# Kernel optimization log

Measured on AMD Instinct MI355X. Metric: run time of the kernel, lower is better.

Reference implementation:

```python
import jax, jax.numpy as jnp
import numpy as np

N_OSC = 2048
N_SAMPLES = 2 ** 14  # hard-coded in the original module
PI = float(np.pi)


def setup_inputs() -> dict:
    key = jax.random.key(0)
    k1, k2 = jax.random.split(key)
    # matches torch.zeros(n_osc, 2).uniform_(0.0001, 0.99999)
    params = jax.random.uniform(k1, (N_OSC, 2), minval=1e-4, maxval=0.99999, dtype=jnp.float32)
    # x is accepted by forward but unused by the math
    x = jax.random.normal(k2, (1, N_SAMPLES), dtype=jnp.float32)
    return {"x": x, "params": params}


def reference(x, params):
    # mode == 'complex':
    #   amp  = ||params||_2 along dim=1  (reassigned BEFORE freq is computed)
    #   freq = angle(amp + i * params[:, 0]) / pi
    amp = jnp.linalg.norm(params, axis=1)                      # (n_osc,)
    freq = jnp.arctan2(params[:, 0], amp) / PI                 # (n_osc,)
    # cumsum of a constant along the sample axis == (i+1) * freq, but we keep
    # the cumsum form to match the original op-for-op.
    accum = jnp.broadcast_to(freq[None, :, None], (1, N_OSC, N_SAMPLES))
    phase = jnp.cumsum(accum, axis=-1) * PI                    # (1, n_osc, n_samples)
    signal = (amp[None, :, None] * jnp.sin(phase)).sum(axis=1)  # (1, n_samples)
    return signal
```

## Files before the change

kernel.cpp:

```cpp
#include <hip/hip_runtime.h>
#include <math.h>

#define N_OSC 2048
#define N_SAMP 16384
#define CHUNKS 16
#define OPC (N_OSC / CHUNKS)

__global__ __launch_bounds__(256) void synth_fused(const float* __restrict__ params,
                                                   float* __restrict__ partial) {
    __shared__ float sh_hi[OPC];
    __shared__ float sh_lo[OPC];
    __shared__ float sh_amp[OPC];

    const int tx = threadIdx.x;
    const int o0 = blockIdx.y * OPC;

    if (tx < OPC) {
        double p0  = (double)params[2 * (o0 + tx) + 0];
        double p1  = (double)params[2 * (o0 + tx) + 1];
        double a   = sqrt(p0 * p0 + p1 * p1);
        double rev = atan2(p0, a) * 0.15915494309189535;
        float hi = (float)rev;
        hi = __uint_as_float(__float_as_uint(hi) & 0xFFFFC000u);
        sh_hi[tx]  = hi;
        sh_lo[tx]  = (float)(rev - (double)hi);
        sh_amp[tx] = (float)a;
    }
    __syncthreads();

    const int s = blockIdx.x * 256 + tx;
    const float sp1 = (float)(s + 1);

    float acc0 = 0.f, acc1 = 0.f;
#pragma unroll 8
    for (int i = 0; i < OPC; i += 2) {
        float uh0 = sp1 * sh_hi[i + 0];
        float uh1 = sp1 * sh_hi[i + 1];
        float t0  = __builtin_amdgcn_fractf(uh0);
        float t1  = __builtin_amdgcn_fractf(uh1);
        float r0  = __builtin_amdgcn_fractf(fmaf(sp1, sh_lo[i + 0], t0));
        float r1  = __builtin_amdgcn_fractf(fmaf(sp1, sh_lo[i + 1], t1));
        acc0 = fmaf(sh_amp[i + 0], __builtin_amdgcn_sinf(r0), acc0);
        acc1 = fmaf(sh_amp[i + 1], __builtin_amdgcn_sinf(r1), acc1);
    }
    partial[blockIdx.y * N_SAMP + s] = acc0 + acc1;
}

__global__ __launch_bounds__(256) void reduce_kernel(const float* __restrict__ partial,
                                                     float* __restrict__ out) {
    int s = blockIdx.x * 256 + threadIdx.x;
    float acc = 0.f;
#pragma unroll
    for (int c = 0; c < CHUNKS; ++c) acc += partial[c * N_SAMP + s];
    out[s] = acc;
}

__global__ __launch_bounds__(256) void inline_kernel(const float* __restrict__ params,
                                                     float* __restrict__ out) {
    int s = blockIdx.x * 256 + threadIdx.x;
    if (s >= N_SAMP) return;
    const double sp1 = (double)(s + 1);
    double acc = 0.0;
    for (int o = 0; o < N_OSC; ++o) {
        double p0 = (double)params[2 * o + 0];
        double p1 = (double)params[2 * o + 1];
        double a  = sqrt(p0 * p0 + p1 * p1);
        double u  = sp1 * (atan2(p0, a) * 0.15915494309189535);
        float  r  = (float)(u - floor(u));
        acc += a * (double)__builtin_amdgcn_sinf(r);
    }
    out[s] = (float)acc;
}

extern "C" void kernel_launch(void* const* d_in, const int* in_sizes, int n_in,
                              void* d_out, int out_size, void* d_ws, size_t ws_size,
                              hipStream_t stream) {
    const float* params = (const float*)d_in[1];
    float* out = (float*)d_out;

    const size_t part_bytes = (size_t)CHUNKS * N_SAMP * sizeof(float);

    if (ws_size >= part_bytes) {
        float* partial = (float*)d_ws;
        synth_fused<<<dim3(N_SAMP / 256, CHUNKS), 256, 0, stream>>>(params, partial);
        reduce_kernel<<<N_SAMP / 256, 256, 0, stream>>>(partial, out);
    } else {
        inline_kernel<<<N_SAMP / 256, 256, 0, stream>>>(params, out);
    }
}
```

Measured before the change: 14.15 us.

## Fuse chunked synthesis and reduction into one kernel with fp32 phase

Replaces the two-kernel scheme (partial sums to workspace, then a reduce kernel) with one kernel where 16 oscillator chunks per block reduce through shared memory. Oscillator phase increments are computed in fp32 per block for all oscillators instead of double with a hi/lo split. This drops a launch, the partial-buffer traffic, and one fract/fma per oscillator, at the cost of redundant per-block atan2 setup and reduced phase accuracy for large sample indices.

```diff
diff --git a/kernel.cpp b/kernel.cpp
--- a/kernel.cpp
+++ b/kernel.cpp
@@ -3,73 +3,55 @@
 
 #define N_OSC 2048
 #define N_SAMP 16384
-#define CHUNKS 16
-#define OPC (N_OSC / CHUNKS)
+#define NCHUNK 16
+#define OPC (N_OSC / NCHUNK)
+#define SPB 64
+#define NTHREADS (NCHUNK * SPB)
 
-__global__ __launch_bounds__(256) void synth_fused(const float* __restrict__ params,
-                                                   float* __restrict__ partial) {
-    __shared__ float sh_hi[OPC];
-    __shared__ float sh_lo[OPC];
-    __shared__ float sh_amp[OPC];
+__global__ __launch_bounds__(NTHREADS) void synth_one(const float* __restrict__ params,
+                                                      float* __restrict__ out) {
+    __shared__ alignas(16) float2 sh[N_OSC];
+    __shared__ float red[NCHUNK][SPB];
 
-    const int tx = threadIdx.x;
-    const int o0 = blockIdx.y * OPC;
+    const int tid = threadIdx.x;
 
-    if (tx < OPC) {
-        double p0  = (double)params[2 * (o0 + tx) + 0];
-        double p1  = (double)params[2 * (o0 + tx) + 1];
-        double a   = sqrt(p0 * p0 + p1 * p1);
-        double rev = atan2(p0, a) * 0.15915494309189535;
-        float hi = (float)rev;
-        hi = __uint_as_float(__float_as_uint(hi) & 0xFFFFC000u);
-        sh_hi[tx]  = hi;
-        sh_lo[tx]  = (float)(rev - (double)hi);
-        sh_amp[tx] = (float)a;
+    {
+        int o = tid;
+        float p0 = params[2 * o], p1 = params[2 * o + 1];
+        float a  = sqrtf(fmaf(p0, p0, p1 * p1));
+        sh[o] = make_float2(atan2f(p0, a) * 0.15915494309189535f, a);
+        o = tid + NTHREADS;
+        p0 = params[2 * o]; p1 = params[2 * o + 1];
+        a  = sqrtf(fmaf(p0, p0, p1 * p1));
+        sh[o] = make_float2(atan2f(p0, a) * 0.15915494309189535f, a);
     }
     __syncthreads();
 
-    const int s = blockIdx.x * 256 + tx;
+    const int chunk = tid >> 6;
+    const int sl    = tid & 63;
+    const int s     = blockIdx.x * SPB + sl;
     const float sp1 = (float)(s + 1);
 
-    float acc0 = 0.f, acc1 = 0.f;
+    const float4* op4 = reinterpret_cast<const float4*>(&sh[chunk * OPC]);
+    float acc0 = 0.f, acc1 = 0.f, acc2 = 0.f, acc3 = 0.f;
 #pragma unroll 8
-    for (int i = 0; i < OPC; i += 2) {
-        float uh0 = sp1 * sh_hi[i + 0];
-        float uh1 = sp1 * sh_hi[i + 1];
-        float t0  = __builtin_amdgcn_fractf(uh0);
-        float t1  = __builtin_amdgcn_fractf(uh1);
-        float r0  = __builtin_amdgcn_fractf(fmaf(sp1, sh_lo[i + 0], t0));
-        float r1  = __builtin_amdgcn_fractf(fmaf(sp1, sh_lo[i + 1], t1));
-        acc0 = fmaf(sh_amp[i + 0], __builtin_amdgcn_sinf(r0), acc0);
-        acc1 = fmaf(sh_amp[i + 1], __builtin_amdgcn_sinf(r1), acc1);
+    for (int i = 0; i < OPC / 2; i += 2) {
+        float4 a = op4[i];
+        float4 b = op4[i + 1];
+        acc0 = fmaf(a.y, __builtin_amdgcn_sinf(__builtin_amdgcn_fractf(sp1 * a.x)), acc0);
+        acc1 = fmaf(a.w, __builtin_amdgcn_sinf(__builtin_amdgcn_fractf(sp1 * a.z)), acc1);
+        acc2 = fmaf(b.y, __builtin_amdgcn_sinf(__builtin_amdgcn_fractf(sp1 * b.x)), acc2);
+        acc3 = fmaf(b.w, __builtin_amdgcn_sinf(__builtin_amdgcn_fractf(sp1 * b.z)), acc3);
     }
-    partial[blockIdx.y * N_SAMP + s] = acc0 + acc1;
-}
+    red[chunk][sl] = (acc0 + acc1) + (acc2 + acc3);
+    __syncthreads();
 
-__global__ __launch_bounds__(256) void reduce_kernel(const float* __restrict__ partial,
-                                                     float* __restrict__ out) {
-    int s = blockIdx.x * 256 + threadIdx.x;
-    float acc = 0.f;
+    if (tid < SPB) {
+        float a = 0.f;
 #pragma unroll
-    for (int c = 0; c < CHUNKS; ++c) acc += partial[c * N_SAMP + s];
-    out[s] = acc;
-}
-
-__global__ __launch_bounds__(256) void inline_kernel(const float* __restrict__ params,
-                                                     float* __restrict__ out) {
-    int s = blockIdx.x * 256 + threadIdx.x;
-    if (s >= N_SAMP) return;
-    const double sp1 = (double)(s + 1);
-    double acc = 0.0;
-    for (int o = 0; o < N_OSC; ++o) {
-        double p0 = (double)params[2 * o + 0];
-        double p1 = (double)params[2 * o + 1];
-        double a  = sqrt(p0 * p0 + p1 * p1);
-        double u  = sp1 * (atan2(p0, a) * 0.15915494309189535);
-        float  r  = (float)(u - floor(u));
-        acc += a * (double)__builtin_amdgcn_sinf(r);
+        for (int c = 0; c < NCHUNK; ++c) a += red[c][tid];
+        out[blockIdx.x * SPB + tid] = a;
     }
-    out[s] = (float)acc;
 }
 
 extern "C" void kernel_launch(void* const* d_in, const int* in_sizes, int n_in,
@@ -77,14 +59,5 @@
                               hipStream_t stream) {
     const float* params = (const float*)d_in[1];
     float* out = (float*)d_out;
-
-    const size_t part_bytes = (size_t)CHUNKS * N_SAMP * sizeof(float);
-
-    if (ws_size >= part_bytes) {
-        float* partial = (float*)d_ws;
-        synth_fused<<<dim3(N_SAMP / 256, CHUNKS), 256, 0, stream>>>(params, partial);
-        reduce_kernel<<<N_SAMP / 256, 256, 0, stream>>>(partial, out);
-    } else {
-        inline_kernel<<<N_SAMP / 256, 256, 0, stream>>>(params, out);
-    }
+    synth_one<<<N_SAMP / SPB, NTHREADS, 0, stream>>>(params, out);
 }
```

After: 12.15 us. 14.2% less time.
